# Kernel optimization log

Hardware: AMD Instinct MI355X
Metric: run time of the kernel (lower is better)

The kernel has to match this reference:

```python
import jax, jax.numpy as jnp
import numpy as np
import math

B, S, DQ, DK, DV, H = 8, 2048, 256, 256, 256, 4
DH = DV // H
EPS = 1e-5

def _layernorm(x, g, b):
    mu = jnp.mean(x, axis=-1, keepdims=True)
    var = jnp.mean(jnp.square(x - mu), axis=-1, keepdims=True)
    return (x - mu) * jax.lax.rsqrt(var + EPS) * g + b

def setup_inputs() -> dict:
    key = jax.random.key(0)
    ks = jax.random.split(key, 12)
    s_in = 1.0 / math.sqrt(DQ)
    s_v = 1.0 / math.sqrt(DV)
    return {
        "Q": jax.random.normal(ks[0], (B, S, DQ), dtype=jnp.float32),
        "K": jax.random.normal(ks[1], (B, S, DK), dtype=jnp.float32),
        "Wq": jax.random.uniform(ks[2], (DQ, DV), jnp.float32, -s_in, s_in),
        "bq": jax.random.uniform(ks[3], (DV,), jnp.float32, -s_in, s_in),
        "Wk": jax.random.uniform(ks[4], (DK, DV), jnp.float32, -s_in, s_in),
        "bk": jax.random.uniform(ks[5], (DV,), jnp.float32, -s_in, s_in),
        "Wv": jax.random.uniform(ks[6], (DK, DV), jnp.float32, -s_in, s_in),
        "bv": jax.random.uniform(ks[7], (DV,), jnp.float32, -s_in, s_in),
        "Wo": jax.random.uniform(ks[8], (DV, DV), jnp.float32, -s_v, s_v),
        "bo": jax.random.uniform(ks[9], (DV,), jnp.float32, -s_v, s_v),
        "g0": jnp.ones((DV,), jnp.float32),
        "beta0": jnp.zeros((DV,), jnp.float32),
        "g1": jnp.ones((DV,), jnp.float32),
        "beta1": jnp.zeros((DV,), jnp.float32),
    }

def reference(Q, K, Wq, bq, Wk, bk, Wv, bv, Wo, bo, g0, beta0, g1, beta1):
    q = Q @ Wq + bq                    # [B,S,DV]
    k = K @ Wk + bk
    v = K @ Wv + bv
    q4 = q.reshape(B, S, H, DH)
    k4 = k.reshape(B, S, H, DH)
    v4 = v.reshape(B, S, H, DH)
    scores = jnp.einsum('bqhd,bkhd->bhqk', q4, k4) / math.sqrt(DH)
    A = jax.nn.softmax(scores, axis=-1)
    o = q4 + jnp.einsum('bhqk,bkhd->bqhd', A, v4)  # residual with projected Q per head
    O = o.reshape(B, S, DV)
    O = _layernorm(O, g0, beta0)
    O = O + jax.nn.relu(O @ Wo + bo)
    O = _layernorm(O, g1, beta1)
    return O
```

## Files before the change

kernel.cpp:

```cpp
#include <hip/hip_runtime.h>
#include <hip/hip_bf16.h>
#include <stdint.h>

typedef uint16_t u16;
typedef uint32_t u32;
typedef __attribute__((ext_vector_type(8))) short short8;
typedef __attribute__((ext_vector_type(4))) float f32x4;

#define LOG2E 1.44269504088896340736f

__device__ __forceinline__ u16 f2bf(float f) {
    u32 u = __builtin_bit_cast(u32, f);
    return (u16)((u + 0x7fffu + ((u >> 16) & 1u)) >> 16);
}
__device__ __forceinline__ float bf2f(u16 h) {
    u32 u = ((u32)h) << 16;
    return __builtin_bit_cast(float, u);
}
__device__ __forceinline__ u32 pack_bf16(float lo, float hi) {
    return (u32)f2bf(lo) | ((u32)f2bf(hi) << 16);
}
__device__ __forceinline__ u32 pack_bf16_fast(float lo, float hi) {
    u32 a = __builtin_bit_cast(u32, lo) + 0x8000u;
    u32 b = __builtin_bit_cast(u32, hi) + 0x8000u;
    return (a >> 16) | (b & 0xffff0000u);
}

__global__ void wt_kernel(const float* __restrict__ Wq, const float* __restrict__ Wk,
                          const float* __restrict__ Wv, const float* __restrict__ Wo,
                          const float* __restrict__ bk, u16* __restrict__ WT,
                          float* __restrict__ bks) {
    const int wsel = blockIdx.y, k = blockIdx.x, n = threadIdx.x;
    const float* W = (wsel == 0) ? Wq : (wsel == 1) ? Wk : (wsel == 2) ? Wv : Wo;
    const float scale = (wsel == 1) ? (0.125f * LOG2E) : 1.0f;
    WT[(size_t)wsel * 65536 + (size_t)n * 256 + k] = f2bf(W[(size_t)k * 256 + n] * scale);
    if (wsel == 1 && k == 0) bks[n] = bk[n] * (0.125f * LOG2E);
}

__global__ __launch_bounds__(256)
void proj_kernel(const float* __restrict__ Qf, const float* __restrict__ Kf,
                 const u16* __restrict__ WT, const float* __restrict__ bq,
                 const float* __restrict__ bks, const float* __restrict__ bvv,
                 u16* __restrict__ qb, u16* __restrict__ kbuf, u16* __restrict__ vbuf) {
    const int z = blockIdx.y;
    const float* Af = (z == 0) ? Qf : Kf;
    const u16* BT = WT + z * 65536;
    const float* bias = (z == 0) ? bq : (z == 1) ? bks : bvv;
    u16* out = (z == 0) ? qb : (z == 1) ? kbuf : vbuf;

    __shared__ u16 As[64 * 64];
    __shared__ u16 Bs[256 * 64];
    const int tid = threadIdx.x;
    const int w = tid >> 6, lane = tid & 63;
    const int g = lane >> 4, lo = lane & 15;
    const int rowB = blockIdx.x * 64;
    const int wc = w * 64;

    const f32x4 fz = {0.f, 0.f, 0.f, 0.f};
    f32x4 acc[4][4];
#pragma unroll
    for (int m = 0; m < 4; ++m)
#pragma unroll
        for (int n = 0; n < 4; ++n) acc[m][n] = fz;

    const int arow = tid & 63, aqtr = tid >> 6;

#pragma unroll 1
    for (int kt = 0; kt < 4; ++kt) {
        const int k0 = kt * 64;
        __syncthreads();
        {
            const float* ga = Af + (size_t)(rowB + arow) * 256 + k0 + aqtr * 16;
            float4 x0 = *(const float4*)ga;
            float4 x1 = *(const float4*)(ga + 4);
            float4 x2 = *(const float4*)(ga + 8);
            float4 x3 = *(const float4*)(ga + 12);
            uint4 pa0, pa1;
            pa0.x = pack_bf16(x0.x, x0.y); pa0.y = pack_bf16(x0.z, x0.w);
            pa0.z = pack_bf16(x1.x, x1.y); pa0.w = pack_bf16(x1.z, x1.w);
            pa1.x = pack_bf16(x2.x, x2.y); pa1.y = pack_bf16(x2.z, x2.w);
            pa1.z = pack_bf16(x3.x, x3.y); pa1.w = pack_bf16(x3.z, x3.w);
            const u32 swA = (u32)((arow & 7) << 4);
            const u32 baA = (u32)(arow * 128 + aqtr * 32);
            *(uint4*)((char*)As + ((baA) ^ swA))      = pa0;
            *(uint4*)((char*)As + ((baA + 16) ^ swA)) = pa1;
            const u16* gb = BT + (size_t)tid * 256 + k0;
            const u32 swB = (u32)((tid & 7) << 4);
            const u32 baB = (u32)(tid * 128);
#pragma unroll
            for (int j = 0; j < 8; ++j) {
                uint4 bj = *(const uint4*)(gb + j * 8);
                *(uint4*)((char*)Bs + ((baB + j * 16) ^ swB)) = bj;
            }
        }
        __syncthreads();
#pragma unroll
        for (int c = 0; c < 2; ++c) {
            short8 af[4], bfr[4];
#pragma unroll
            for (int m = 0; m < 4; ++m) {
                const int row = m * 16 + lo;
                const u32 addr = (u32)(row * 128 + c * 64 + g * 16) ^ (u32)((row & 7) << 4);
                af[m] = *(const short8*)((char*)As + addr);
            }
#pragma unroll
            for (int n = 0; n < 4; ++n) {
                const int row = wc + n * 16 + lo;
                const u32 addr = (u32)(row * 128 + c * 64 + g * 16) ^ (u32)((row & 7) << 4);
                bfr[n] = *(const short8*)((char*)Bs + addr);
            }
#pragma unroll
            for (int m = 0; m < 4; ++m)
#pragma unroll
                for (int n = 0; n < 4; ++n)
                    acc[m][n] = __builtin_amdgcn_mfma_f32_16x16x32_bf16(af[m], bfr[n], acc[m][n], 0, 0, 0);
        }
    }

    float bv[4];
#pragma unroll
    for (int n = 0; n < 4; ++n) bv[n] = bias[wc + n * 16 + lo];
#pragma unroll
    for (int m = 0; m < 4; ++m)
#pragma unroll
        for (int r = 0; r < 4; ++r) {
            const size_t row = (size_t)(rowB + m * 16 + g * 4 + r);
#pragma unroll
            for (int n = 0; n < 4; ++n)
                out[row * 256 + wc + n * 16 + lo] = f2bf(acc[m][n][r] + bv[n]);
        }
}

__global__ __launch_bounds__(512, 4)
void attn_kernel(const u16* __restrict__ qb, const u16* __restrict__ kb,
                 const u16* __restrict__ vb, u16* __restrict__ Ob) {
    __shared__ u16 Klds[2 * 64 * 64];
    __shared__ u16 Vtlds[2 * 64 * 64];
    __shared__ u16 Plds[8 * 16 * 64];
    const int tid = threadIdx.x;
    const int w = tid >> 6, lane = tid & 63;
    const int g = lane >> 4, lo = lane & 15;
    const int bid = blockIdx.x;
    const int xcd = bid & 7;
    const int member = (bid >> 3) & 15;
    const int grp = ((bid >> 7) << 3) | xcd;
    const int q0 = member * 128;
    const int h = grp & 3, b = grp >> 2;
    const size_t hbase = (size_t)b * 2048 * 256 + (size_t)h * 64;

    short8 qf[2];
#pragma unroll
    for (int c = 0; c < 2; ++c) {
        const size_t row = (size_t)(q0 + w * 16 + lo);
        qf[c] = *(const short8*)&qb[hbase + row * 256 + c * 32 + g * 8];
    }
    const short8 vones = {0x3F80, 0x3F80, 0x3F80, 0x3F80, 0x3F80, 0x3F80, 0x3F80, 0x3F80};

    const f32x4 fz = {0.f, 0.f, 0.f, 0.f};
    f32x4 oacc[4];
#pragma unroll
    for (int n = 0; n < 4; ++n) oacc[n] = fz;
    f32x4 l_acc = fz;
    float m_run = -1e30f;

    char* Pb = (char*)Plds + w * 2048;

    const bool kRole = (tid < 256);
    const int skey = tid & 63, sseg = (tid >> 6) & 3;
    const int t4 = tid & 255;
    const int vkey = (t4 & 31) * 2, vd0 = (t4 >> 5) * 8;
    const u16* gbase;
    int goff2;
    if (kRole) { gbase = &kb[hbase + (size_t)skey * 256 + sseg * 16]; goff2 = 8; }
    else       { gbase = &vb[hbase + (size_t)vkey * 256 + vd0];       goff2 = 256; }

    uint4 s0, s1;
    auto load_tile = [&](int kt) {
        const u16* p = gbase + (size_t)kt * 16384;
        s0 = *(const uint4*)p;
        s1 = *(const uint4*)(p + goff2);
    };
    auto write_tile = [&](int sel) {
        if (kRole) {
            char* Kb_ = (char*)Klds + sel * 8192;
            const u32 sw = (u32)((skey & 7) << 4);
            const u32 ba = (u32)(skey * 128 + sseg * 32);
            *(uint4*)(Kb_ + ((ba) ^ sw)) = s0;
            *(uint4*)(Kb_ + ((ba + 16) ^ sw)) = s1;
        } else {
            char* Vb_ = (char*)Vtlds + sel * 8192;
            union { uint4 v; u16 hh[8]; } a0, a1;
            a0.v = s0; a1.v = s1;
#pragma unroll
            for (int i = 0; i < 8; ++i) {
                const int d = vd0 + i;
                const u32 addr = (u32)(d * 128 + vkey * 2) ^ (u32)((d & 7) << 4);
                *(u32*)(Vb_ + addr) = (u32)a0.hh[i] | ((u32)a1.hh[i] << 16);
            }
        }
    };

    load_tile(0);
    write_tile(0);
    load_tile(1);
    __syncthreads();

#pragma unroll 1
    for (int kt = 0; kt < 32; ++kt) {
        const int cur = kt & 1;
        char* Klb = (char*)Klds + cur * 8192;
        char* Vtb = (char*)Vtlds + cur * 8192;

        f32x4 sc[4];
#pragma unroll
        for (int km = 0; km < 4; ++km) sc[km] = fz;
        __builtin_amdgcn_s_setprio(1);
#pragma unroll
        for (int c = 0; c < 2; ++c)
#pragma unroll
            for (int km = 0; km < 4; ++km) {
                const int key = km * 16 + lo;
                const u32 addr = (u32)(key * 128 + c * 64 + g * 16) ^ (u32)((key & 7) << 4);
                const short8 kf = *(const short8*)(Klb + addr);
                sc[km] = __builtin_amdgcn_mfma_f32_16x16x32_bf16(kf, qf[c], sc[km], 0, 0, 0);
            }
        __builtin_amdgcn_s_setprio(0);

        float mt = -1e30f;
#pragma unroll
        for (int km = 0; km < 4; ++km)
#pragma unroll
            for (int r = 0; r < 4; ++r) mt = fmaxf(mt, sc[km][r]);
        mt = fmaxf(mt, __shfl_xor(mt, 16));
        mt = fmaxf(mt, __shfl_xor(mt, 32));
        if (!__all(mt <= m_run + 11.5f)) {
            const float mnew = fmaxf(m_run, mt);
            const float alpha = __builtin_amdgcn_exp2f(m_run - mnew);
#pragma unroll
            for (int r = 0; r < 4; ++r) {
                const float a = __shfl(alpha, (lane & 48) | (g * 4 + r));
                l_acc[r] *= a;
#pragma unroll
                for (int n = 0; n < 4; ++n) oacc[n][r] *= a;
            }
            m_run = mnew;
        }
#pragma unroll
        for (int km = 0; km < 4; ++km)
#pragma unroll
            for (int r = 0; r < 4; ++r)
                sc[km][r] = __builtin_amdgcn_exp2f(sc[km][r] - m_run);

        {
            const u32 sw = (u32)((lo & 7) << 4);
#pragma unroll
            for (int km = 0; km < 4; ++km) {
                uint2 val;
                val.x = pack_bf16_fast(sc[km][0], sc[km][1]);
                val.y = pack_bf16_fast(sc[km][2], sc[km][3]);
                const u32 addr = (u32)(lo * 128 + km * 32 + g * 8) ^ sw;
                *(uint2*)(Pb + addr) = val;
            }
        }

        __builtin_amdgcn_s_setprio(1);
#pragma unroll
        for (int c = 0; c < 2; ++c) {
            const u32 paddr = (u32)(lo * 128 + c * 64 + g * 16) ^ (u32)((lo & 7) << 4);
            const short8 pf = *(const short8*)(Pb + paddr);
#pragma unroll
            for (int n = 0; n < 4; ++n) {
                const int d = n * 16 + lo;
                const u32 addr = (u32)(d * 128 + c * 64 + g * 16) ^ (u32)((d & 7) << 4);
                const short8 vf = *(const short8*)(Vtb + addr);
                oacc[n] = __builtin_amdgcn_mfma_f32_16x16x32_bf16(pf, vf, oacc[n], 0, 0, 0);
            }
            l_acc = __builtin_amdgcn_mfma_f32_16x16x32_bf16(pf, vones, l_acc, 0, 0, 0);
        }
        __builtin_amdgcn_s_setprio(0);

        if (kt < 31) write_tile(cur ^ 1);
        if (kt < 30) load_tile(kt + 2);
        __syncthreads();
    }

#pragma unroll
    for (int r = 0; r < 4; ++r) {
        const float li = 1.0f / l_acc[r];
        const size_t row = (size_t)(q0 + w * 16 + g * 4 + r);
#pragma unroll
        for (int n = 0; n < 4; ++n) {
            const int d = n * 16 + lo;
            const size_t idx = hbase + row * 256 + d;
            Ob[idx] = f2bf(oacc[n][r] * li + bf2f(qb[idx]));
        }
    }
}

__global__ __launch_bounds__(256)
void tail_kernel(const u16* __restrict__ Ob, const u16* __restrict__ BT,
                 const float* __restrict__ bo, const float* __restrict__ g0,
                 const float* __restrict__ be0, const float* __restrict__ g1,
                 const float* __restrict__ be1, float* __restrict__ out) {
    __shared__ char lds[49152];
    char* Xs = lds;
    u16* Bs = (u16*)(lds + 16384);
    const int tid = threadIdx.x;
    const int w = tid >> 6, lane = tid & 63;
    const int g = lane >> 4, lo = lane & 15;
    const int rowB = blockIdx.x * 32;
    const int wc = w * 64;

    const int lrow = tid >> 3, lseg = tid & 7;
    const u32 lsw = (u32)((lrow & 7) << 4);

    {
        const u16* gb = BT + (size_t)tid * 256;
        const u32 swB = (u32)((tid & 7) << 4);
        const u32 baB = (u32)(tid * 128);
#pragma unroll
        for (int j = 0; j < 8; ++j) {
            uint4 bj = *(const uint4*)(gb + j * 8);
            *(uint4*)((char*)Bs + ((baB + j * 16) ^ swB)) = bj;
        }
    }

    {
        const size_t grow = (size_t)(rowB + lrow);
        const u16* src = Ob + grow * 256 + lseg * 32;
        uint4 r4[4];
#pragma unroll
        for (int j = 0; j < 4; ++j) r4[j] = *(const uint4*)(src + j * 8);
        float s = 0.f, q = 0.f;
#pragma unroll
        for (int j = 0; j < 4; ++j) {
            const u32 uu[4] = {r4[j].x, r4[j].y, r4[j].z, r4[j].w};
#pragma unroll
            for (int e = 0; e < 4; ++e) {
                const float f0 = bf2f((u16)(uu[e] & 0xffff));
                const float f1 = bf2f((u16)(uu[e] >> 16));
                s += f0 + f1;
                q += f0 * f0 + f1 * f1;
            }
        }
        s += __shfl_xor(s, 1); q += __shfl_xor(q, 1);
        s += __shfl_xor(s, 2); q += __shfl_xor(q, 2);
        s += __shfl_xor(s, 4); q += __shfl_xor(q, 4);
        const float mu = s * (1.f / 256.f);
        const float var = q * (1.f / 256.f) - mu * mu;
        const float rstd = rsqrtf(var + 1e-5f);
        const float* gp = g0 + lseg * 32;
        const float* bp = be0 + lseg * 32;
#pragma unroll
        for (int j = 0; j < 4; ++j) {
            const u32 uu[4] = {r4[j].x, r4[j].y, r4[j].z, r4[j].w};
            float4 gv0 = *(const float4*)(gp + j * 8);
            float4 gv1 = *(const float4*)(gp + j * 8 + 4);
            float4 bb0 = *(const float4*)(bp + j * 8);
            float4 bb1 = *(const float4*)(bp + j * 8 + 4);
            uint4 o;
            o.x = pack_bf16((bf2f((u16)(uu[0] & 0xffff)) - mu) * rstd * gv0.x + bb0.x,
                            (bf2f((u16)(uu[0] >> 16))    - mu) * rstd * gv0.y + bb0.y);
            o.y = pack_bf16((bf2f((u16)(uu[1] & 0xffff)) - mu) * rstd * gv0.z + bb0.z,
                            (bf2f((u16)(uu[1] >> 16))    - mu) * rstd * gv0.w + bb0.w);
            o.z = pack_bf16((bf2f((u16)(uu[2] & 0xffff)) - mu) * rstd * gv1.x + bb1.x,
                            (bf2f((u16)(uu[2] >> 16))    - mu) * rstd * gv1.y + bb1.y);
            o.w = pack_bf16((bf2f((u16)(uu[3] & 0xffff)) - mu) * rstd * gv1.z + bb1.z,
                            (bf2f((u16)(uu[3] >> 16))    - mu) * rstd * gv1.w + bb1.w);
            const u32 addr = (u32)(lrow * 512 + lseg * 64 + j * 16) ^ lsw;
            *(uint4*)(Xs + addr) = o;
        }
    }
    __syncthreads();

    const f32x4 fz = {0.f, 0.f, 0.f, 0.f};
    f32x4 acc[2][4];
#pragma unroll
    for (int m = 0; m < 2; ++m)
#pragma unroll
        for (int n = 0; n < 4; ++n) acc[m][n] = fz;

#pragma unroll 1
    for (int kt = 0; kt < 4; ++kt) {
        if (kt) {
            __syncthreads();
            const u16* gb = BT + (size_t)tid * 256 + kt * 64;
            const u32 swB = (u32)((tid & 7) << 4);
            const u32 baB = (u32)(tid * 128);
#pragma unroll
            for (int j = 0; j < 8; ++j) {
                uint4 bj = *(const uint4*)(gb + j * 8);
                *(uint4*)((char*)Bs + ((baB + j * 16) ^ swB)) = bj;
            }
            __syncthreads();
        }
#pragma unroll
        for (int c = 0; c < 2; ++c) {
            short8 af[2], bfr[4];
#pragma unroll
            for (int m = 0; m < 2; ++m) {
                const int row = m * 16 + lo;
                const u32 addr = (u32)(row * 512 + kt * 128 + c * 64 + g * 16) ^ (u32)((row & 7) << 4);
                af[m] = *(const short8*)(Xs + addr);
            }
#pragma unroll
            for (int n = 0; n < 4; ++n) {
                const int row = wc + n * 16 + lo;
                const u32 addr = (u32)(row * 128 + c * 64 + g * 16) ^ (u32)((row & 7) << 4);
                bfr[n] = *(const short8*)((char*)Bs + addr);
            }
#pragma unroll
            for (int m = 0; m < 2; ++m)
#pragma unroll
                for (int n = 0; n < 4; ++n)
                    acc[m][n] = __builtin_amdgcn_mfma_f32_16x16x32_bf16(af[m], bfr[n], acc[m][n], 0, 0, 0);
        }
    }

    float bv[4];
#pragma unroll
    for (int n = 0; n < 4; ++n) bv[n] = bo[wc + n * 16 + lo];

    __syncthreads();

#pragma unroll
    for (int m = 0; m < 2; ++m)
#pragma unroll
        for (int r = 0; r < 4; ++r) {
            const int row_l = m * 16 + g * 4 + r;
            const u32 sw = (u32)((row_l & 7) << 4);
#pragma unroll
            for (int n = 0; n < 4; ++n) {
                const int col = wc + n * 16 + lo;
                const u32 badr = (u32)(row_l * 512 + col * 2);
                char* p = Xs + ((badr & ~15u) ^ sw) + (badr & 15u);
                const float resid = bf2f(*(u16*)p);
                *(u16*)p = f2bf(resid + fmaxf(acc[m][n][r] + bv[n], 0.f));
            }
        }
    __syncthreads();

    {
        const u32 rbase = (u32)(lrow * 512 + lseg * 64);
        float s = 0.f, q = 0.f;
#pragma unroll
        for (int j = 0; j < 4; ++j) {
            uint4 v4 = *(const uint4*)(Xs + ((rbase + j * 16) ^ lsw));
            const u32 uu[4] = {v4.x, v4.y, v4.z, v4.w};
#pragma unroll
            for (int e = 0; e < 4; ++e) {
                const float f0 = bf2f((u16)(uu[e] & 0xffff));
                const float f1 = bf2f((u16)(uu[e] >> 16));
                s += f0 + f1;
                q += f0 * f0 + f1 * f1;
            }
        }
        s += __shfl_xor(s, 1); q += __shfl_xor(q, 1);
        s += __shfl_xor(s, 2); q += __shfl_xor(q, 2);
        s += __shfl_xor(s, 4); q += __shfl_xor(q, 4);
        const float mu = s * (1.f / 256.f);
        const float var = q * (1.f / 256.f) - mu * mu;
        const float rstd = rsqrtf(var + 1e-5f);
        const size_t grow = (size_t)(rowB + lrow);
        float* op = out + grow * 256 + lseg * 32;
        const float* gp = g1 + lseg * 32;
        const float* bp = be1 + lseg * 32;
#pragma unroll
        for (int j = 0; j < 4; ++j) {
            uint4 v4 = *(const uint4*)(Xs + ((rbase + j * 16) ^ lsw));
            const u32 uu[4] = {v4.x, v4.y, v4.z, v4.w};
#pragma unroll
            for (int e = 0; e < 2; ++e) {
                float4 gv = *(const float4*)(gp + j * 8 + e * 4);
                float4 bb = *(const float4*)(bp + j * 8 + e * 4);
                float4 o4;
                o4.x = (bf2f((u16)(uu[e * 2]     & 0xffff)) - mu) * rstd * gv.x + bb.x;
                o4.y = (bf2f((u16)(uu[e * 2]     >> 16))    - mu) * rstd * gv.y + bb.y;
                o4.z = (bf2f((u16)(uu[e * 2 + 1] & 0xffff)) - mu) * rstd * gv.z + bb.z;
                o4.w = (bf2f((u16)(uu[e * 2 + 1] >> 16))    - mu) * rstd * gv.w + bb.w;
                *(float4*)(op + j * 8 + e * 4) = o4;
            }
        }
    }
}

extern "C" void kernel_launch(void* const* d_in, const int* in_sizes, int n_in,
                              void* d_out, int out_size, void* d_ws, size_t ws_size,
                              hipStream_t stream) {
    const float* Q  = (const float*)d_in[0];
    const float* K  = (const float*)d_in[1];
    const float* Wq = (const float*)d_in[2];
    const float* bq = (const float*)d_in[3];
    const float* Wk = (const float*)d_in[4];
    const float* bk = (const float*)d_in[5];
    const float* Wv = (const float*)d_in[6];
    const float* bv = (const float*)d_in[7];
    const float* Wo = (const float*)d_in[8];
    const float* bo = (const float*)d_in[9];
    const float* g0 = (const float*)d_in[10];
    const float* be0 = (const float*)d_in[11];
    const float* g1 = (const float*)d_in[12];
    const float* be1 = (const float*)d_in[13];
    float* out = (float*)d_out;

    const size_t NE = (size_t)8 * 2048 * 256;
    char* ws = (char*)d_ws;
    size_t off = 0;
    auto alloc = [&](size_t bytes) { char* p = ws + off; off += (bytes + 255) & ~(size_t)255; return p; };
    u16* qb   = (u16*)alloc(NE * 2);
    u16* kbuf = (u16*)alloc(NE * 2);
    u16* vbuf = (u16*)alloc(NE * 2);
    u16* WT   = (u16*)alloc(4 * 65536 * 2);
    float* bks = (float*)alloc(256 * 4);
    u16* Ob16 = (u16*)alloc(NE * 2);

    wt_kernel<<<dim3(256, 4), 256, 0, stream>>>(Wq, Wk, Wv, Wo, bk, WT, bks);

    proj_kernel<<<dim3(256, 3), 256, 0, stream>>>(Q, K, WT, bq, bks, bv, qb, kbuf, vbuf);

    attn_kernel<<<512, 512, 0, stream>>>(qb, kbuf, vbuf, Ob16);

    tail_kernel<<<512, 256, 0, stream>>>(Ob16, WT + 3 * 65536, bo, g0, be0, g1, be1, out);
}
```

Measured before the change: 113.0 us.

## Halve attention block size to 64 queries and 4 warps, doubling grid

Shrinks each attention block from 8 waves and 128 query rows to 4 waves and 64 query rows, and launches twice as many blocks. Every thread now loads and stages both K and V tile pieces instead of splitting the roles between halves of the block. The intent is better occupancy and load balance across CUs, with less LDS per block. The cost is that each K/V tile is reused by fewer query rows, so global K/V traffic doubles and each thread does more staging work.

```diff
diff --git a/kernel.cpp b/kernel.cpp
--- a/kernel.cpp
+++ b/kernel.cpp
@@ -131,20 +131,20 @@
         }
 }
 
-__global__ __launch_bounds__(512, 4)
+__global__ __launch_bounds__(256, 4)
 void attn_kernel(const u16* __restrict__ qb, const u16* __restrict__ kb,
                  const u16* __restrict__ vb, u16* __restrict__ Ob) {
     __shared__ u16 Klds[2 * 64 * 64];
     __shared__ u16 Vtlds[2 * 64 * 64];
-    __shared__ u16 Plds[8 * 16 * 64];
+    __shared__ u16 Plds[4 * 16 * 64];
     const int tid = threadIdx.x;
     const int w = tid >> 6, lane = tid & 63;
     const int g = lane >> 4, lo = lane & 15;
     const int bid = blockIdx.x;
     const int xcd = bid & 7;
-    const int member = (bid >> 3) & 15;
-    const int grp = ((bid >> 7) << 3) | xcd;
-    const int q0 = member * 128;
+    const int member = (bid >> 3) & 31;
+    const int grp = ((bid >> 8) << 3) | xcd;
+    const int q0 = member * 64;
     const int h = grp & 3, b = grp >> 2;
     const size_t hbase = (size_t)b * 2048 * 256 + (size_t)h * 64;
 
@@ -165,38 +165,34 @@
 
     char* Pb = (char*)Plds + w * 2048;
 
-    const bool kRole = (tid < 256);
-    const int skey = tid & 63, sseg = (tid >> 6) & 3;
-    const int t4 = tid & 255;
-    const int vkey = (t4 & 31) * 2, vd0 = (t4 >> 5) * 8;
-    const u16* gbase;
-    int goff2;
-    if (kRole) { gbase = &kb[hbase + (size_t)skey * 256 + sseg * 16]; goff2 = 8; }
-    else       { gbase = &vb[hbase + (size_t)vkey * 256 + vd0];       goff2 = 256; }
-
-    uint4 s0, s1;
+    const int skey = tid & 63, sseg = tid >> 6;
+    const int vkey = (tid & 31) * 2, vd0 = (tid >> 5) * 8;
+    const u16* gk = &kb[hbase + (size_t)skey * 256 + sseg * 16];
+    const u16* gv = &vb[hbase + (size_t)vkey * 256 + vd0];
+
+    uint4 k0s, k1s, v0s, v1s;
     auto load_tile = [&](int kt) {
-        const u16* p = gbase + (size_t)kt * 16384;
-        s0 = *(const uint4*)p;
-        s1 = *(const uint4*)(p + goff2);
+        const u16* pk = gk + (size_t)kt * 16384;
+        k0s = *(const uint4*)pk;
+        k1s = *(const uint4*)(pk + 8);
+        const u16* pv = gv + (size_t)kt * 16384;
+        v0s = *(const uint4*)pv;
+        v1s = *(const uint4*)(pv + 256);
     };
     auto write_tile = [&](int sel) {
-        if (kRole) {
-            char* Kb_ = (char*)Klds + sel * 8192;
-            const u32 sw = (u32)((skey & 7) << 4);
-            const u32 ba = (u32)(skey * 128 + sseg * 32);
-            *(uint4*)(Kb_ + ((ba) ^ sw)) = s0;
-            *(uint4*)(Kb_ + ((ba + 16) ^ sw)) = s1;
-        } else {
-            char* Vb_ = (char*)Vtlds + sel * 8192;
-            union { uint4 v; u16 hh[8]; } a0, a1;
-            a0.v = s0; a1.v = s1;
-#pragma unroll
-            for (int i = 0; i < 8; ++i) {
-                const int d = vd0 + i;
-                const u32 addr = (u32)(d * 128 + vkey * 2) ^ (u32)((d & 7) << 4);
-                *(u32*)(Vb_ + addr) = (u32)a0.hh[i] | ((u32)a1.hh[i] << 16);
-            }
+        char* Kb_ = (char*)Klds + sel * 8192;
+        const u32 sw = (u32)((skey & 7) << 4);
+        const u32 ba = (u32)(skey * 128 + sseg * 32);
+        *(uint4*)(Kb_ + ((ba) ^ sw)) = k0s;
+        *(uint4*)(Kb_ + ((ba + 16) ^ sw)) = k1s;
+        char* Vb_ = (char*)Vtlds + sel * 8192;
+        union { uint4 v; u16 hh[8]; } a0, a1;
+        a0.v = v0s; a1.v = v1s;
+#pragma unroll
+        for (int i = 0; i < 8; ++i) {
+            const int d = vd0 + i;
+            const u32 addr = (u32)(d * 128 + vkey * 2) ^ (u32)((d & 7) << 4);
+            *(u32*)(Vb_ + addr) = (u32)a0.hh[i] | ((u32)a1.hh[i] << 16);
         }
     };
 
@@ -518,7 +514,7 @@
 
     proj_kernel<<<dim3(256, 3), 256, 0, stream>>>(Q, K, WT, bq, bks, bv, qb, kbuf, vbuf);
 
-    attn_kernel<<<512, 512, 0, stream>>>(qb, kbuf, vbuf, Ob16);
+    attn_kernel<<<1024, 256, 0, stream>>>(qb, kbuf, vbuf, Ob16);
 
     tail_kernel<<<512, 256, 0, stream>>>(Ob16, WT + 3 * 65536, bo, g0, be0, g1, be1, out);
 }
```

After: 131.3 us. +16.2%, slower.

## Split attention key range in two and merge partials in a combine kernel

Applied to the files above, without the earlier changes.

Splits each attention work item's 32 key tiles into two halves handled by separate blocks (1024 blocks instead of 512). Each block writes unnormalized-by-other-half partial outputs plus running max and sum. A new combine kernel merges them with log-sum-exp weights and adds the Q residual. The aim is more parallelism and better CU occupancy on the 256-CU part, at the cost of an extra kernel launch and extra HBM traffic for the partials.

```diff
diff --git a/kernel.cpp b/kernel.cpp
--- a/kernel.cpp
+++ b/kernel.cpp
@@ -133,7 +133,8 @@
 
 __global__ __launch_bounds__(512, 4)
 void attn_kernel(const u16* __restrict__ qb, const u16* __restrict__ kb,
-                 const u16* __restrict__ vb, u16* __restrict__ Ob) {
+                 const u16* __restrict__ vb, u16* __restrict__ On,
+                 float2* __restrict__ ml) {
     __shared__ u16 Klds[2 * 64 * 64];
     __shared__ u16 Vtlds[2 * 64 * 64];
     __shared__ u16 Plds[8 * 16 * 64];
@@ -143,10 +144,12 @@
     const int bid = blockIdx.x;
     const int xcd = bid & 7;
     const int member = (bid >> 3) & 15;
-    const int grp = ((bid >> 7) << 3) | xcd;
+    const int ch = (bid >> 7) & 1;
+    const int grp = ((bid >> 8) << 3) | xcd;
     const int q0 = member * 128;
     const int h = grp & 3, b = grp >> 2;
     const size_t hbase = (size_t)b * 2048 * 256 + (size_t)h * 64;
+    const size_t NE = (size_t)8 * 2048 * 256;
 
     short8 qf[2];
 #pragma unroll
@@ -200,13 +203,14 @@
         }
     };
 
-    load_tile(0);
+    const int kt0 = ch * 16, kt1 = kt0 + 16;
+    load_tile(kt0);
     write_tile(0);
-    load_tile(1);
+    load_tile(kt0 + 1);
     __syncthreads();
 
 #pragma unroll 1
-    for (int kt = 0; kt < 32; ++kt) {
+    for (int kt = kt0; kt < kt1; ++kt) {
         const int cur = kt & 1;
         char* Klb = (char*)Klds + cur * 8192;
         char* Vtb = (char*)Vtlds + cur * 8192;
@@ -279,22 +283,55 @@
         }
         __builtin_amdgcn_s_setprio(0);
 
-        if (kt < 31) write_tile(cur ^ 1);
-        if (kt < 30) load_tile(kt + 2);
+        if (kt < kt1 - 1) write_tile(cur ^ 1);
+        if (kt < kt1 - 2) load_tile(kt + 2);
         __syncthreads();
     }
 
 #pragma unroll
     for (int r = 0; r < 4; ++r) {
         const float li = 1.0f / l_acc[r];
-        const size_t row = (size_t)(q0 + w * 16 + g * 4 + r);
+        const float mrow = __shfl(m_run, (lane & 48) | (g * 4 + r));
+        const int rloc = q0 + w * 16 + g * 4 + r;
+        const size_t row = (size_t)rloc;
 #pragma unroll
         for (int n = 0; n < 4; ++n) {
             const int d = n * 16 + lo;
-            const size_t idx = hbase + row * 256 + d;
-            Ob[idx] = f2bf(oacc[n][r] * li + bf2f(qb[idx]));
-        }
-    }
+            On[(size_t)ch * NE + hbase + row * 256 + d] = f2bf(oacc[n][r] * li);
+        }
+        if (lo == 0)
+            ml[((size_t)ch * 32 + grp) * 2048 + rloc] = make_float2(mrow, l_acc[r]);
+    }
+}
+
+__global__ __launch_bounds__(256)
+void comb_kernel(const u16* __restrict__ On, const float2* __restrict__ ml,
+                 const u16* __restrict__ qb, u16* __restrict__ Ob) {
+    const int w = threadIdx.x >> 6, lane = threadIdx.x & 63;
+    const int g = lane >> 4;
+    const int row_s = blockIdx.x * 4 + w;
+    const int b = row_s >> 11, q = row_s & 2047;
+    const size_t NE = (size_t)8 * 2048 * 256;
+    const int grp = b * 4 + g;
+
+    const float2 ml1 = ml[(size_t)grp * 2048 + q];
+    const float2 ml2 = ml[(size_t)(32 + grp) * 2048 + q];
+    const float M = fmaxf(ml1.x, ml2.x);
+    float w1 = ml1.y * __builtin_amdgcn_exp2f(ml1.x - M);
+    float w2 = ml2.y * __builtin_amdgcn_exp2f(ml2.x - M);
+    const float inv = 1.0f / (w1 + w2);
+    w1 *= inv; w2 *= inv;
+
+    const size_t idx = (size_t)row_s * 256 + lane * 4;
+    const uint2 a1 = *(const uint2*)(On + idx);
+    const uint2 a2 = *(const uint2*)(On + NE + idx);
+    const uint2 qv = *(const uint2*)(qb + idx);
+    uint2 o;
+    o.x = pack_bf16(w1 * bf2f((u16)(a1.x & 0xffff)) + w2 * bf2f((u16)(a2.x & 0xffff)) + bf2f((u16)(qv.x & 0xffff)),
+                    w1 * bf2f((u16)(a1.x >> 16))    + w2 * bf2f((u16)(a2.x >> 16))    + bf2f((u16)(qv.x >> 16)));
+    o.y = pack_bf16(w1 * bf2f((u16)(a1.y & 0xffff)) + w2 * bf2f((u16)(a2.y & 0xffff)) + bf2f((u16)(qv.y & 0xffff)),
+                    w1 * bf2f((u16)(a1.y >> 16))    + w2 * bf2f((u16)(a2.y >> 16))    + bf2f((u16)(qv.y >> 16)));
+    *(uint2*)(Ob + idx) = o;
 }
 
 __global__ __launch_bounds__(256)
@@ -513,12 +550,16 @@
     u16* WT   = (u16*)alloc(4 * 65536 * 2);
     float* bks = (float*)alloc(256 * 4);
     u16* Ob16 = (u16*)alloc(NE * 2);
+    u16* On   = (u16*)alloc(NE * 2 * 2);
+    float2* ml = (float2*)alloc(2 * 32 * 2048 * sizeof(float2));
 
     wt_kernel<<<dim3(256, 4), 256, 0, stream>>>(Wq, Wk, Wv, Wo, bk, WT, bks);
 
     proj_kernel<<<dim3(256, 3), 256, 0, stream>>>(Q, K, WT, bq, bks, bv, qb, kbuf, vbuf);
 
-    attn_kernel<<<512, 512, 0, stream>>>(qb, kbuf, vbuf, Ob16);
+    attn_kernel<<<1024, 512, 0, stream>>>(qb, kbuf, vbuf, On, ml);
+
+    comb_kernel<<<4096, 256, 0, stream>>>(On, ml, qb, Ob16);
 
     tail_kernel<<<512, 256, 0, stream>>>(Ob16, WT + 3 * 65536, bo, g0, be0, g1, be1, out);
 }
```

Result: slower. 122.3 us (+8.3%).
